# Kernel tuning notes

Measured on AMD Instinct MI355X. Metric: run time of the kernel, lower is better.

The kernel has to match this reference:

```python
import jax, jax.numpy as jnp
import numpy as np

KS = 3          # deformable kernel size
PAD = 1         # padding (kernel_size // 2)
EPS = 1e-5      # BatchNorm eps


def conv2d(x, w, b):
    # plain 3x3 conv, stride 1, pad 1, NCHW / OIHW
    y = jax.lax.conv_general_dilated(x, w, window_strides=(1, 1),
                                     padding=[(PAD, PAD), (PAD, PAD)],
                                     dimension_numbers=("NCHW", "OIHW", "NCHW"))
    return y + b[None, :, None, None]


def deform_conv(x, offset, mask, w, b):
    # modulated deformable conv v2 (torchvision deform_conv2d semantics)
    B, C, H, W = x.shape
    K = KS * KS
    ky, kx = jnp.meshgrid(jnp.arange(KS), jnp.arange(KS), indexing="ij")
    ky = ky.reshape(-1).astype(x.dtype)
    kx = kx.reshape(-1).astype(x.dtype)
    off = offset.reshape(B, K, 2, H, W)          # channel order: (dy, dx) per kernel tap
    dy, dx = off[:, :, 0], off[:, :, 1]          # [B,K,H,W]
    py = dy + (ky - PAD)[None, :, None, None] + jnp.arange(H, dtype=x.dtype)[None, None, :, None]
    px = dx + (kx - PAD)[None, :, None, None] + jnp.arange(W, dtype=x.dtype)[None, None, None, :]
    y0 = jnp.floor(py); x0 = jnp.floor(px)
    ly = py - y0; lx = px - x0
    y0i = y0.astype(jnp.int32); x0i = x0.astype(jnp.int32)
    y1i = y0i + 1; x1i = x0i + 1
    xf = x.reshape(B, C, H * W)

    def gather(yi, xi):
        valid = (yi >= 0) & (yi < H) & (xi >= 0) & (xi < W)          # zero padding outside
        idx = jnp.clip(yi, 0, H - 1) * W + jnp.clip(xi, 0, W - 1)    # [B,K,H,W]
        g = jax.vmap(lambda xb, ib: jnp.take(xb, ib, axis=1))(xf, idx.reshape(B, -1))
        g = g.reshape(B, C, K, H, W)
        return g * valid[:, None].astype(x.dtype)

    v = (gather(y0i, x0i) * ((1 - ly) * (1 - lx))[:, None]
         + gather(y0i, x1i) * ((1 - ly) * lx)[:, None]
         + gather(y1i, x0i) * (ly * (1 - lx))[:, None]
         + gather(y1i, x1i) * (ly * lx)[:, None])                    # [B,C,K,H,W]
    v = v * mask[:, None]                                            # modulation
    out = jnp.einsum("bckhw,ock->bohw", v, w.reshape(w.shape[0], C, K))
    return out + b[None, :, None, None]


def setup_inputs() -> dict:
    key = jax.random.key(0)
    ks = jax.random.split(key, 5)
    B, Cin, Cout, H, W = 8, 64, 64, 128, 128
    K = KS * KS
    x = jax.random.normal(ks[0], (B, Cin, H, W), jnp.float32)
    off_w = jax.random.normal(ks[1], (2 * K, Cin, KS, KS), jnp.float32) * 0.01
    off_b = jnp.zeros((2 * K,), jnp.float32)
    mod_w = jax.random.normal(ks[2], (K, Cin, KS, KS), jnp.float32) * 0.01
    mod_b = jnp.zeros((K,), jnp.float32)
    w = jax.random.normal(ks[3], (Cout, Cin, KS, KS), jnp.float32) * (1.0 / np.sqrt(Cin * K))
    b = jnp.zeros((Cout,), jnp.float32)
    gamma = jnp.ones((Cout,), jnp.float32)
    beta = jnp.zeros((Cout,), jnp.float32)
    return {"x": x, "off_w": off_w, "off_b": off_b, "mod_w": mod_w,
            "mod_b": mod_b, "w": w, "b": b, "gamma": gamma, "beta": beta}


def reference(x, off_w, off_b, mod_w, mod_b, w, b, gamma, beta):
    offset = conv2d(x, off_w, off_b)                       # [B,2K,H,W]
    mask = 2.0 * jax.nn.sigmoid(conv2d(x, mod_w, mod_b))   # [B,K,H,W]
    y = deform_conv(x, offset, mask, w, b)                 # [B,Cout,H,W]
    # BatchNorm2d (training-mode batch stats, biased variance)
    mean = y.mean(axis=(0, 2, 3), keepdims=True)
    var = y.var(axis=(0, 2, 3), keepdims=True)
    yn = (y - mean) / jnp.sqrt(var + EPS)
    yn = gamma[None, :, None, None] * yn + beta[None, :, None, None]
    return jax.nn.relu(yn)
```

## Files before the change

### kernel.cpp

```cpp
#include <hip/hip_runtime.h>
#include <math.h>

#define Hn 128
#define Wn 128
#define HW 16384
#define NPIX 131072
#define EPSv 1e-5f

#define XT_OFF   0
#define WBTA_OFF 4194304
#define WBTB_OFF 4204544
#define STAT_OFF 4225024


typedef short s16x8 __attribute__((ext_vector_type(8)));
typedef unsigned short u16x4 __attribute__((ext_vector_type(4)));
typedef float f32x4 __attribute__((ext_vector_type(4)));
typedef unsigned int u32x4 __attribute__((ext_vector_type(4)));

__device__ __forceinline__ unsigned short f2bf(float f) {
  unsigned u = __float_as_uint(f);
  return (unsigned short)((u + 0x7fffu + ((u >> 16) & 1u)) >> 16);
}
__device__ __forceinline__ float bf2f(unsigned short s) {
  return __uint_as_float((unsigned)s << 16);
}
__device__ __forceinline__ unsigned cvt_pk_bf16(float lo, float hi) {
  unsigned r;
  asm("v_cvt_pk_bf16_f32 %0, %1, %2" : "=v"(r) : "v"(lo), "v"(hi));
  return r;
}

__global__ __launch_bounds__(256) void prep_xform_kernel(
    const float* __restrict__ x, unsigned short* __restrict__ xt,
    const float* __restrict__ off_w, const float* __restrict__ mod_w,
    const float* __restrict__ w, unsigned short* __restrict__ wbtA,
    unsigned short* __restrict__ wbtB, float* __restrict__ stat) {
  int blk = blockIdx.x;
  if (blk < 512) {
    int b = blk & 7;
    int hw = ((blk >> 3) << 8) + threadIdx.x;
    const float* xb = x + ((size_t)(b << 6) << 14) + hw;
    unsigned short* o = xt + (((size_t)(b << 14)) + hw) * 64;
#pragma unroll
    for (int g = 0; g < 8; ++g) {
      float v[8];
#pragma unroll
      for (int j = 0; j < 8; ++j) v[j] = xb[(size_t)((g << 3) + j) << 14];
      s16x8 pk;
#pragma unroll
      for (int j = 0; j < 8; ++j) pk[j] = (short)f2bf(v[j]);
      *(s16x8*)(o + (g << 3)) = pk;
    }
    return;
  }
  int i = ((blk - 512) << 8) + threadIdx.x;
  if (i < 1024) stat[i] = 0.f;
  if (i < 20480) {
    int e = i & 31, oc = (i >> 5) & 31, it = i >> 10;
    int tp = it % 5, chunk = it / 5;
    int tap = tp * 2 + (e >> 4);
    int c = (chunk << 4) + (e & 15);
    float v = 0.f;
    if (tap < 9) {
      if (oc < 18) v = off_w[(oc * 64 + c) * 9 + tap];
      else if (oc < 27) v = mod_w[((oc - 18) * 64 + c) * 9 + tap];
    }
    wbtA[i] = f2bf(v);
  } else if (i < 20480 + 40960) {
    int j = i - 20480;
    int j3 = j & 7;
    int l = (j >> 3) & 63;
    int nt = (j >> 9) & 3;
    int it = j >> 11;
    int tp = it % 5, chunk = it / 5;
    int tap = tp * 2 + (l >> 5);
    int c = (chunk << 4) + (((l >> 4) & 1) << 3) + j3;
    int oc = (nt << 4) + (l & 15);
    float v = (tap < 9) ? w[(oc * 64 + c) * 9 + tap] : 0.f;
    wbtB[j] = f2bf(v);
  }
}

__global__ __launch_bounds__(256, 4) void fused_dconv_kernel(
    const unsigned short* __restrict__ xt, const unsigned short* __restrict__ wbtA,
    const unsigned short* __restrict__ wbtB,
    const float* __restrict__ off_b, const float* __restrict__ mod_b,
    const float* __restrict__ bias, float* __restrict__ y,
    float* __restrict__ stat) {
  __shared__ float offm[27 * 128];
  __shared__ unsigned short geow[9 * 128 * 4];
  __shared__ unsigned short geoi[9 * 128];
  __shared__ unsigned short stage[3 * 128 * 16];
  int t = threadIdx.x;
  int bx = blockIdx.x;
  int b = bx & 7, h = bx >> 3;
  int lane = t & 63, wv = t >> 6;
  int ln = lane & 15, quad = (lane >> 4) & 3;
  int hw = h << 7;

  const unsigned short* xtb = xt + ((size_t)(b << 14)) * 64;

  {
    int p0 = (wv << 5) + ln, p1 = p0 + 16;
    int s_ = quad >> 1, cj = (quad & 1) << 3;
    f32x4 acc1[2][2];
#pragma unroll
    for (int mt = 0; mt < 2; ++mt)
#pragma unroll
      for (int nt = 0; nt < 2; ++nt) acc1[mt][nt] = (f32x4){0.f, 0.f, 0.f, 0.f};

    for (int chunk = 0; chunk < 4; ++chunk) {
      for (int q = t; q < 768; q += 256) {
        int row = q >> 8;
        int rem = q & 255;
        int px = rem >> 1;
        int half = rem & 1;
        int gy = h - 1 + row;
        s16x8 v = (s16x8){0, 0, 0, 0, 0, 0, 0, 0};
        if (gy >= 0 && gy < Hn)
          v = *(const s16x8*)(xtb + ((size_t)(gy << 7)) * 64 + (px << 6) + (chunk << 4) + (half << 3));
        *(s16x8*)(stage + (q << 3)) = v;
      }
      __syncthreads();

#pragma unroll
      for (int tp = 0; tp < 5; ++tp) {
        int it = chunk * 5 + tp;
        int tap = tp * 2 + s_;
        s16x8 B0 = (s16x8){0, 0, 0, 0, 0, 0, 0, 0};
        s16x8 B1 = (s16x8){0, 0, 0, 0, 0, 0, 0, 0};
        if (tap < 9) {
          const unsigned short* rowl = stage + (tap / 3) * 2048 + cj;
          int gx0 = p0 + tap % 3 - 1;
          int gx1 = p1 + tap % 3 - 1;
          if (gx0 >= 0 && gx0 < Wn) B0 = *(const s16x8*)(rowl + (gx0 << 4));
          if (gx1 >= 0 && gx1 < Wn) B1 = *(const s16x8*)(rowl + (gx1 << 4));
        }
#pragma unroll
        for (int mt = 0; mt < 2; ++mt) {
          s16x8 A = *(const s16x8*)(wbtA + (size_t)((it << 5) + (mt << 4) + ln) * 32 + (quad << 3));
          acc1[mt][0] = __builtin_amdgcn_mfma_f32_16x16x32_bf16(A, B0, acc1[mt][0], 0, 0, 0);
          acc1[mt][1] = __builtin_amdgcn_mfma_f32_16x16x32_bf16(A, B1, acc1[mt][1], 0, 0, 0);
        }
      }
      __syncthreads();
    }

#pragma unroll
    for (int mt = 0; mt < 2; ++mt)
#pragma unroll
      for (int r = 0; r < 4; ++r) {
        int oc = (mt << 4) + (quad << 2) + r;
#pragma unroll
        for (int nt = 0; nt < 2; ++nt) {
          int px = (wv << 5) + (nt << 4) + ln;
          float val = acc1[mt][nt][r];
          if (oc < 18) {
            offm[(oc << 7) + px] = val + off_b[oc];
          } else if (oc < 27) {
            float z = val + mod_b[oc - 18];
            offm[(oc << 7) + px] = 2.f / (1.f + expf(-z));
          }
        }
      }
  }
  __syncthreads();

  for (int i = t; i < 1152; i += 256) {
    int tap = i >> 7, p2 = i & 127;
    float dy = offm[((2 * tap) << 7) + p2];
    float dx = offm[((2 * tap + 1) << 7) + p2];
    float m = offm[((18 + tap) << 7) + p2];
    float py = dy + (float)(h + tap / 3 - 1);
    float pxf = dx + (float)(p2 + tap % 3 - 1);
    float y0f = floorf(py), x0f = floorf(pxf);
    float ly = py - y0f, lx = pxf - x0f;
    int y0 = (int)y0f, x0 = (int)x0f;
    int y1 = y0 + 1, x1 = x0 + 1;
    float fy0 = (y0 >= 0 && y0 < Hn) ? 1.f : 0.f;
    float fy1 = (y1 >= 0 && y1 < Hn) ? 1.f : 0.f;
    float fx0 = (x0 >= 0 && x0 < Wn) ? 1.f : 0.f;
    float fx1 = (x1 >= 0 && x1 < Wn) ? 1.f : 0.f;
    float ax0 = (1.f - lx) * fx0, ax1 = lx * fx1;
    float ay0 = (1.f - ly) * fy0 * m, ay1 = ly * fy1 * m;
    int cy0 = min(max(y0, 0), Hn - 1), cy1 = min(max(y1, 0), Hn - 1);
    int cx0 = min(max(x0, 0), Wn - 1), cx1 = min(max(x1, 0), Wn - 1);
    int cbase = min(cx0, Wn - 2), rbase = min(cy0, Hn - 2);
    float gx0 = (cx0 == cbase ? ax0 : 0.f) + (cx1 == cbase ? ax1 : 0.f);
    float gx1 = (cx0 == cbase + 1 ? ax0 : 0.f) + (cx1 == cbase + 1 ? ax1 : 0.f);
    float gy0 = (cy0 == rbase ? ay0 : 0.f) + (cy1 == rbase ? ay1 : 0.f);
    float gy1 = (cy0 == rbase + 1 ? ay0 : 0.f) + (cy1 == rbase + 1 ? ay1 : 0.f);
    unsigned short* gw = geow + i * 4;
    gw[0] = f2bf(gy0 * gx0);
    gw[1] = f2bf(gy0 * gx1);
    gw[2] = f2bf(gy1 * gx0);
    gw[3] = f2bf(gy1 * gx1);
    geoi[i] = (unsigned short)((rbase << 7) + cbase);
  }
  __syncthreads();

  int l4 = ln;
  int s4 = lane >> 4;
  int tapS = lane >> 5;
  int chalf = s4 & 1;

  f32x4 acc[2][4];
#pragma unroll
  for (int m = 0; m < 2; ++m)
#pragma unroll
    for (int n = 0; n < 4; ++n) acc[m][n] = (f32x4){0.f, 0.f, 0.f, 0.f};

  for (int tp = 0; tp < 5; ++tp) {
    int tap = tp * 2 + tapS;
    bool live = (tap < 9);
    float w00[2], w01[2], w10[2], w11[2];
    const unsigned short* cpb[2];
#pragma unroll
    for (int m = 0; m < 2; ++m) {
      if (live) {
        int px = (wv << 5) + (m << 4) + l4;
        int gidx = (tap << 7) + px;
        u16x4 wq = *(const u16x4*)(geow + gidx * 4);
        unsigned ib = geoi[gidx];
        w00[m] = bf2f(wq[0]);
        w01[m] = bf2f(wq[1]);
        w10[m] = bf2f(wq[2]);
        w11[m] = bf2f(wq[3]);
        cpb[m] = xtb + (size_t)ib * 64 + (chalf << 3);
      } else {
        cpb[m] = xtb;
        w00[m] = w01[m] = w10[m] = w11[m] = 0.f;
      }
    }
#pragma unroll 2
    for (int chunk = 0; chunk < 4; ++chunk) {
      int it = chunk * 5 + tp;
      s16x8 A[2];
#pragma unroll
      for (int m = 0; m < 2; ++m) {
        if (live) {
          const unsigned short* cp = cpb[m] + (chunk << 4);
          s16x8 c00 = *(const s16x8*)(cp);
          s16x8 c01 = *(const s16x8*)(cp + 64);
          s16x8 c10 = *(const s16x8*)(cp + 8192);
          s16x8 c11 = *(const s16x8*)(cp + 8192 + 64);
          u32x4 au;
#pragma unroll
          for (int jj = 0; jj < 4; ++jj) {
            float v0 = w00[m] * bf2f((unsigned short)c00[2 * jj]) +
                       w01[m] * bf2f((unsigned short)c01[2 * jj]) +
                       w10[m] * bf2f((unsigned short)c10[2 * jj]) +
                       w11[m] * bf2f((unsigned short)c11[2 * jj]);
            float v1 = w00[m] * bf2f((unsigned short)c00[2 * jj + 1]) +
                       w01[m] * bf2f((unsigned short)c01[2 * jj + 1]) +
                       w10[m] * bf2f((unsigned short)c10[2 * jj + 1]) +
                       w11[m] * bf2f((unsigned short)c11[2 * jj + 1]);
            au[jj] = cvt_pk_bf16(v0, v1);
          }
          A[m] = __builtin_bit_cast(s16x8, au);
        } else {
          A[m] = (s16x8){0, 0, 0, 0, 0, 0, 0, 0};
        }
      }
      const unsigned short* wb = wbtB + (((size_t)it) << 11) + (lane << 3);
      __builtin_amdgcn_s_setprio(1);
#pragma unroll
      for (int n = 0; n < 4; ++n) {
        s16x8 Bf = *(const s16x8*)(wb + (n << 9));
        acc[0][n] = __builtin_amdgcn_mfma_f32_16x16x32_bf16(A[0], Bf, acc[0][n], 0, 0, 0);
        acc[1][n] = __builtin_amdgcn_mfma_f32_16x16x32_bf16(A[1], Bf, acc[1][n], 0, 0, 0);
      }
      __builtin_amdgcn_s_setprio(0);
    }
  }

  float sac[4], ssc[4];
#pragma unroll
  for (int n = 0; n < 4; ++n) { sac[n] = 0.f; ssc[n] = 0.f; }
#pragma unroll
  for (int m = 0; m < 2; ++m) {
    int px0 = (wv << 5) + (m << 4) + (s4 << 2);
#pragma unroll
    for (int n = 0; n < 4; ++n) {
      int oc = (n << 4) + l4;
      float bv = bias[oc];
      float4 o;
      o.x = acc[m][n][0] + bv;
      o.y = acc[m][n][1] + bv;
      o.z = acc[m][n][2] + bv;
      o.w = acc[m][n][3] + bv;
      sac[n] += o.x + o.y + o.z + o.w;
      ssc[n] += o.x * o.x + o.y * o.y + o.z * o.z + o.w * o.w;
      *(float4*)(y + (((size_t)(b << 6) + oc) << 14) + hw + px0) = o;
    }
  }
#pragma unroll
  for (int n = 0; n < 4; ++n) {
    sac[n] += __shfl_xor(sac[n], 16);
    sac[n] += __shfl_xor(sac[n], 32);
    ssc[n] += __shfl_xor(ssc[n], 16);
    ssc[n] += __shfl_xor(ssc[n], 32);
  }
  if (lane < 16) {
#pragma unroll
    for (int n = 0; n < 4; ++n) {
      int oc = (n << 4) + lane;
      offm[(wv << 6) + oc] = sac[n];
      offm[256 + (wv << 6) + oc] = ssc[n];
    }
  }
  __syncthreads();
  if (t < 64) {
    float S = offm[t] + offm[64 + t] + offm[128 + t] + offm[192 + t];
    float SS = offm[256 + t] + offm[320 + t] + offm[384 + t] + offm[448 + t];
    float* sb = stat + ((bx & 7) << 7);
    atomicAdd(sb + t, S);
    atomicAdd(sb + 64 + t, SS);
  }
}

__global__ __launch_bounds__(256) void bnrelu_kernel(
    float* __restrict__ y, const float* __restrict__ stat,
    const float* __restrict__ gamma, const float* __restrict__ beta) {
  __shared__ float gs[64], bs[64];
  int t = threadIdx.x;
  if (t < 64) {
    float S = 0.f, SS = 0.f;
#pragma unroll
    for (int k = 0; k < 8; ++k) {
      S += stat[(k << 7) + t];
      SS += stat[(k << 7) + 64 + t];
    }
    float mean = S * (1.f / (float)NPIX);
    float var = SS * (1.f / (float)NPIX) - mean * mean;
    float r = rsqrtf(var + EPSv);
    float g = gamma[t] * r;
    gs[t] = g;
    bs[t] = beta[t] - mean * g;
  }
  __syncthreads();
  float4* y4 = (float4*)y;
  for (int i = blockIdx.x * 256 + t; i < 2097152; i += gridDim.x * 256) {
    int c = (i >> 12) & 63;
    float g = gs[c];
    float bt = bs[c];
    float4 v = y4[i];
    v.x = fmaxf(v.x * g + bt, 0.f);
    v.y = fmaxf(v.y * g + bt, 0.f);
    v.z = fmaxf(v.z * g + bt, 0.f);
    v.w = fmaxf(v.w * g + bt, 0.f);
    y4[i] = v;
  }
}

extern "C" void kernel_launch(void* const* d_in, const int* in_sizes, int n_in,
                              void* d_out, int out_size, void* d_ws, size_t ws_size,
                              hipStream_t stream) {
  const float* x     = (const float*)d_in[0];
  const float* off_w = (const float*)d_in[1];
  const float* off_b = (const float*)d_in[2];
  const float* mod_w = (const float*)d_in[3];
  const float* mod_b = (const float*)d_in[4];
  const float* w     = (const float*)d_in[5];
  const float* b     = (const float*)d_in[6];
  const float* gamma = (const float*)d_in[7];
  const float* beta  = (const float*)d_in[8];
  float* out = (float*)d_out;
  float* ws  = (float*)d_ws;

  unsigned short* xt  = (unsigned short*)(ws + XT_OFF);
  unsigned short* wbtA = (unsigned short*)(ws + WBTA_OFF);
  unsigned short* wbtB = (unsigned short*)(ws + WBTB_OFF);
  float* stat  = ws + STAT_OFF;

  prep_xform_kernel<<<752, 256, 0, stream>>>(x, xt, off_w, mod_w, w, wbtA, wbtB, stat);
  fused_dconv_kernel<<<1024, 256, 0, stream>>>(xt, wbtA, wbtB, off_b, mod_b, b, out, stat);
  bnrelu_kernel<<<2048, 256, 0, stream>>>(out, stat, gamma, beta);
}
```

Measured before the change: 201.4 us.

## Double-buffer offset-conv input staging with direct global-to-LDS loads

```diff
diff --git a/kernel.cpp b/kernel.cpp
--- a/kernel.cpp
+++ b/kernel.cpp
@@ -89,9 +89,9 @@
     const float* __restrict__ bias, float* __restrict__ y,
     float* __restrict__ stat) {
   __shared__ float offm[27 * 128];
-  __shared__ unsigned short geow[9 * 128 * 4];
-  __shared__ unsigned short geoi[9 * 128];
-  __shared__ unsigned short stage[3 * 128 * 16];
+  __shared__ unsigned short un[2 * 3 * 128 * 16];
+  unsigned short* geow = un;
+  unsigned short* geoi = un + 4608;
   int t = threadIdx.x;
   int bx = blockIdx.x;
   int b = bx & 7, h = bx >> 3;
@@ -104,26 +104,37 @@
   {
     int p0 = (wv << 5) + ln, p1 = p0 + 16;
     int s_ = quad >> 1, cj = (quad & 1) << 3;
+    int px_s = t >> 1, half_s = t & 1;
+
+    auto STAGE = [&](int buf, int chunk) {
+#pragma unroll
+      for (int k = 0; k < 3; ++k) {
+        int gy = h - 1 + k;
+        unsigned short* lp = un + buf * 6144 + (k << 11) + (wv << 9);
+        if ((unsigned)gy < 128u) {
+          const unsigned short* gp =
+              xtb + ((size_t)gy << 13) + (px_s << 6) + (chunk << 4) + (half_s << 3);
+          __builtin_amdgcn_global_load_lds(
+              (const __attribute__((address_space(1))) unsigned int*)gp,
+              (__attribute__((address_space(3))) unsigned int*)lp, 16, 0, 0);
+        } else {
+          *(s16x8*)(un + buf * 6144 + (k << 11) + (t << 3)) = (s16x8){0, 0, 0, 0, 0, 0, 0, 0};
+        }
+      }
+    };
+
     f32x4 acc1[2][2];
 #pragma unroll
     for (int mt = 0; mt < 2; ++mt)
 #pragma unroll
       for (int nt = 0; nt < 2; ++nt) acc1[mt][nt] = (f32x4){0.f, 0.f, 0.f, 0.f};
 
+    STAGE(0, 0);
+    __syncthreads();
+
     for (int chunk = 0; chunk < 4; ++chunk) {
-      for (int q = t; q < 768; q += 256) {
-        int row = q >> 8;
-        int rem = q & 255;
-        int px = rem >> 1;
-        int half = rem & 1;
-        int gy = h - 1 + row;
-        s16x8 v = (s16x8){0, 0, 0, 0, 0, 0, 0, 0};
-        if (gy >= 0 && gy < Hn)
-          v = *(const s16x8*)(xtb + ((size_t)(gy << 7)) * 64 + (px << 6) + (chunk << 4) + (half << 3));
-        *(s16x8*)(stage + (q << 3)) = v;
-      }
-      __syncthreads();
-
+      if (chunk < 3) STAGE((chunk + 1) & 1, chunk + 1);
+      const unsigned short* sb = un + (chunk & 1) * 6144;
 #pragma unroll
       for (int tp = 0; tp < 5; ++tp) {
         int it = chunk * 5 + tp;
@@ -131,7 +142,7 @@
         s16x8 B0 = (s16x8){0, 0, 0, 0, 0, 0, 0, 0};
         s16x8 B1 = (s16x8){0, 0, 0, 0, 0, 0, 0, 0};
         if (tap < 9) {
-          const unsigned short* rowl = stage + (tap / 3) * 2048 + cj;
+          const unsigned short* rowl = sb + (tap / 3) * 2048 + cj;
           int gx0 = p0 + tap % 3 - 1;
           int gx1 = p1 + tap % 3 - 1;
           if (gx0 >= 0 && gx0 < Wn) B0 = *(const s16x8*)(rowl + (gx0 << 4));
```

Result: no change. 200.9 us, median of 2 (-0.3%).
